# Optimization experiments

Measured on AMD Instinct MI355X. Metric: run time of the kernel, lower is better.

## Reference

```python
import jax, jax.numpy as jnp
import numpy as np

B, N, C_IN, FC0, K = 16, 32768, 32, 256, 1024
CHUNK = 64  # chunk over the K=1024 attention channels to bound the [N,CHUNK,C] intermediate
BN_EPS = 1e-5


def _lengths():
    rng = np.random.default_rng(0)
    r = rng.integers(1024, 3072, size=B)
    l = (r * N) // r.sum()
    l[-1] += N - l.sum()
    assert l.min() > 0 and l.sum() == N
    return jnp.asarray(l, dtype=jnp.int32)


def setup_inputs() -> dict:
    key = jax.random.key(0)
    ks = jax.random.split(key, 16)
    f32 = jnp.float32
    x = jax.random.normal(ks[0], (N, C_IN), dtype=f32)
    # conv1d_1 (1x1 conv == per-point linear), BN1
    w1 = jax.random.normal(ks[1], (FC0, C_IN), dtype=f32) * 0.1
    b1 = jax.random.normal(ks[2], (FC0,), dtype=f32) * 0.1
    g1 = 1.0 + 0.1 * jax.random.normal(ks[3], (FC0,), dtype=f32)
    be1 = 0.1 * jax.random.normal(ks[4], (FC0,), dtype=f32)
    m1 = 0.1 * jax.random.normal(ks[5], (FC0,), dtype=f32)
    v1 = 0.5 + jax.random.uniform(ks[6], (FC0,), dtype=f32)
    # conv1d_2, BN2
    w2 = jax.random.normal(ks[7], (K, FC0), dtype=f32) * 0.05
    b2 = jax.random.normal(ks[8], (K,), dtype=f32) * 0.1
    g2 = 1.0 + 0.1 * jax.random.normal(ks[9], (K,), dtype=f32)
    be2 = 0.1 * jax.random.normal(ks[10], (K,), dtype=f32)
    m2 = 0.1 * jax.random.normal(ks[11], (K,), dtype=f32)
    v2 = 0.5 + jax.random.uniform(ks[12], (K,), dtype=f32)
    # fc_1, BN3
    fcw = jax.random.normal(ks[13], (FC0, C_IN * K), dtype=f32) * 0.01
    fcb = jax.random.normal(ks[14], (FC0,), dtype=f32) * 0.1
    kb = jax.random.split(ks[15], 4)
    g3 = 1.0 + 0.1 * jax.random.normal(kb[0], (FC0,), dtype=f32)
    be3 = 0.1 * jax.random.normal(kb[1], (FC0,), dtype=f32)
    m3 = 0.1 * jax.random.normal(kb[2], (FC0,), dtype=f32)
    v3 = 0.5 + jax.random.uniform(kb[3], (FC0,), dtype=f32)
    return dict(x=x, length=_lengths(), w1=w1, b1=b1, g1=g1, be1=be1, m1=m1, v1=v1,
                w2=w2, b2=b2, g2=g2, be2=be2, m2=m2, v2=v2,
                fcw=fcw, fcb=fcb, g3=g3, be3=be3, m3=m3, v3=v3)


def _bn(x, g, b, m, v):
    # eval-mode BatchNorm (running stats)
    return (x - m) * (g * jax.lax.rsqrt(v + BN_EPS)) + b


def _forward(x, length, w1, b1, g1, be1, m1, v1, w2, b2, g2, be2, m2, v2,
             fcw, fcb, g3, be3, m3, v3):
    # attention features: conv1x1 -> BN -> ReLU, twice  -> [N, K]
    att = jax.nn.relu(_bn(x @ w1.T + b1, g1, be1, m1, v1))
    att = jax.nn.relu(_bn(att @ w2.T + b2, g2, be2, m2, v2))

    seg = jnp.repeat(jnp.arange(B, dtype=jnp.int32), length, total_repeat_length=N)  # [N]

    # per-segment softmax over the point axis (torch F.softmax(..., dim=0))
    mx = jax.ops.segment_max(att, seg, num_segments=B)              # [B, K]
    e = jnp.exp(att - mx[seg])
    w = e / jax.ops.segment_sum(e, seg, num_segments=B)[seg]        # [N, K]

    # per-segment weighted pooling: out[b] = att_b.T @ x_b, chunked over K
    chunks = []
    for s in range(0, K, CHUNK):
        contrib = w[:, s:s + CHUNK, None] * x[:, None, :]           # [N, CHUNK, C]
        chunks.append(jax.ops.segment_sum(contrib, seg, num_segments=B))
    pooled = jnp.concatenate(chunks, axis=1)                        # [B, K, C]
    pooled = pooled / length[:, None, None].astype(x.dtype)
    out2 = pooled.reshape(B, K * C_IN)                              # row-major flatten of [K, C]

    r = _bn(out2 @ fcw.T + fcb, g3, be3, m3, v3)                    # [B, 256]
    # F.normalize(p=2, dim=1, eps=1e-12)
    return r / jnp.maximum(jnp.linalg.norm(r, axis=1, keepdims=True), 1e-12)


def reference(x, length, w1, b1, g1, be1, m1, v1, w2, b2, g2, be2, m2, v2,
              fcw, fcb, g3, be3, m3, v3):
    return _forward(x, length, w1, b1, g1, be1, m1, v1, w2, b2, g2, be2, m2, v2,
                    fcw, fcb, g3, be3, m3, v3)
```

## Files before the change

### kernel.cpp

```cpp
#include <hip/hip_runtime.h>
#include <hip/hip_bf16.h>

typedef __bf16 bf16x8 __attribute__((ext_vector_type(8)));
typedef unsigned short u16x8 __attribute__((ext_vector_type(8)));
typedef float f32x4 __attribute__((ext_vector_type(4)));
typedef unsigned long long ull;

__device__ inline unsigned short f2bf(float f) {
    unsigned u = __builtin_bit_cast(unsigned, f);
    unsigned r = (u + 0x7fffu + ((u >> 16) & 1u)) >> 16;
    return (unsigned short)r;
}
__device__ inline float bf2f(unsigned short h) {
    unsigned u = ((unsigned)h) << 16;
    return __builtin_bit_cast(float, u);
}

__device__ inline void gload_lds16(const void* g, void* l) {
    __builtin_amdgcn_global_load_lds((const __attribute__((address_space(1))) void*)g,
                                     (__attribute__((address_space(3))) void*)l, 16, 0, 0);
}

#define MAXCH 272

__global__ __launch_bounds__(256) void k01_prep_gemm1(const float* __restrict__ x,
                                                      const float* __restrict__ w1,
                                                      const float* __restrict__ b1,
                                                      const float* __restrict__ g1,
                                                      const float* __restrict__ be1,
                                                      const float* __restrict__ m1,
                                                      const float* __restrict__ v1,
                                                      const float* __restrict__ w2,
                                                      const int* __restrict__ length,
                                                      unsigned short* __restrict__ w2p,
                                                      int* __restrict__ meta,
                                                      unsigned short* __restrict__ att1) {
    int tid = threadIdx.x;
    int i = blockIdx.x * 256 + tid;
    if (i < 32768) {
        int kb = i >> 9, kk = (i >> 6) & 7, l = i & 63;
        int col = kb * 16 + (l & 15);
        int kin = kk * 32 + (l >> 4) * 8;
        unsigned short v[8];
#pragma unroll
        for (int j = 0; j < 8; j++) v[j] = f2bf(w2[(size_t)col * 256 + kin + j]);
        *(ull*)(w2p + (size_t)i * 8)     = *(ull*)&v[0];
        *(ull*)(w2p + (size_t)i * 8 + 4) = *(ull*)&v[4];
    }
    if (blockIdx.x == 0 && tid < 64) {
        int lane = tid;
        int b = lane & 15;
        int len = length[b];
        int off = 0, chbase = 0, nch = 0;
        int nchb = (len + 127) >> 7;
#pragma unroll
        for (int j = 0; j < 16; j++) {
            int lj = __shfl(len, j, 64);
            int nj = __shfl(nchb, j, 64);
            if (j < b) { off += lj; chbase += nj; }
            nch += nj;
        }
        int total = __shfl(off + len, 15, 64);
        if (lane < 16) {
            meta[b] = off;
            meta[848 + b] = chbase;
            meta[864 + b] = chbase + nchb;
            if (b == 0) { meta[16] = total; meta[17] = nch; }
            for (int t = 0; t < nchb; t++) {
                int s = off + t * 128;
                int en = off + len < s + 128 ? off + len : s + 128;
                meta[304 + chbase + t] = s;
                meta[576 + chbase + t] = en;
            }
        }
    }
    __shared__ float xs[64][33];
    int row0 = blockIdx.x * 64;
    for (int ii = tid; ii < 64 * 32; ii += 256) {
        int rr = ii >> 5, c = ii & 31;
        xs[rr][c] = x[(row0 + rr) * 32 + c];
    }
    __syncthreads();
    int j = tid;
    float w[32];
#pragma unroll
    for (int c = 0; c < 32; c++) w[c] = w1[j * 32 + c];
    float s = g1[j] * rsqrtf(v1[j] + 1e-5f);
    float bias = (b1[j] - m1[j]) * s + be1[j];
    for (int rr = 0; rr < 64; rr++) {
        float acc = 0.f;
#pragma unroll
        for (int c = 0; c < 32; c++) acc = fmaf(xs[rr][c], w[c], acc);
        float t = fmaf(acc, s, bias);
        att1[(row0 + rr) * 256 + j] = f2bf(fmaxf(t, 0.f));
    }
}

__global__ __launch_bounds__(256, 2) void k23_fused(const unsigned short* __restrict__ att1,
                                                    const unsigned short* __restrict__ w2p,
                                                    const float* __restrict__ x,
                                                    const int* __restrict__ meta,
                                                    const float* __restrict__ b2,
                                                    const float* __restrict__ g2,
                                                    const float* __restrict__ be2,
                                                    const float* __restrict__ m2,
                                                    const float* __restrict__ v2,
                                                    unsigned short* __restrict__ pP,
                                                    float* __restrict__ pS) {
    __shared__ __align__(16) unsigned short As[2][128 * 64];
    __shared__ __align__(16) unsigned short xT[48 * 128];
    int flat = blockIdx.x;
    int xcd = flat & 7, q = flat >> 3;
    int ch = (q >> 3) * 8 + xcd;
    int kt = q & 7;
    if (ch >= meta[17]) return;
    int n0 = meta[304 + ch];
    int rows = meta[576 + ch] - n0;
    int col0 = kt * 128;
    int tid = threadIdx.x, lane = tid & 63, wave = tid >> 6;
    int lr = lane & 15, s16 = lane >> 4;
    int wr = wave >> 1, wc = wave & 1;

    auto stage = [&](int t, int buf) {
#pragma unroll
        for (int it = 0; it < 4; it++) {
            int idx = it * 256 + tid;
            int row = idx >> 3, slot = idx & 7;
            int srow = row < rows ? row : rows - 1;
            int g = slot ^ (row & 7);
            gload_lds16(att1 + (size_t)(n0 + srow) * 256 + t * 64 + g * 8,
                        (char*)As + buf * 16384 + it * 4096 + wave * 1024);
        }
    };

    int kb0 = kt * 8 + wc * 4;
    auto loadB = [&](int t, bf16x8 (&bb)[2][4]) {
#pragma unroll
        for (int kk = 0; kk < 2; kk++)
#pragma unroll
            for (int n = 0; n < 4; n++)
                bb[kk][n] = *(const bf16x8*)(const void*)(
                    w2p + (size_t)(((kb0 + n) * 8 + t * 2 + kk) * 64 + lane) * 8);
    };

    bf16x8 b0[2][4], b1[2][4];
    stage(0, 0);
    loadB(0, b0);

#pragma unroll
    for (int p = 0; p < 8; p++) {
        int nb = p * 16 + (tid >> 5) * 2;
        int c = tid & 31;
        float v0 = (nb < rows) ? x[(size_t)(n0 + nb) * 32 + c] : 0.f;
        float v1 = (nb + 1 < rows) ? x[(size_t)(n0 + nb + 1) * 32 + c] : 0.f;
        unsigned pk = ((unsigned)f2bf(v1) << 16) | f2bf(v0);
        int byte = c * 256 + ((nb * 2) ^ ((c & 15) << 4));
        *(unsigned*)((char*)xT + byte) = pk;
    }
    if (tid < 128) {
        int byte = 32 * 256 + tid * 2;
        *(unsigned short*)((char*)xT + byte) = (tid < rows) ? f2bf(1.f) : (unsigned short)0;
    }
    __syncthreads();

    f32x4 acc[4][4] = {};
#pragma unroll
    for (int t = 0; t < 4; t++) {
        if (t < 3) stage(t + 1, (t & 1) ^ 1);
        if (t == 0) loadB(1, b1);
        else if (t == 1) loadB(2, b0);
        else if (t == 2) loadB(3, b1);
        const char* Ab = (const char*)As + (t & 1) * 16384;
#pragma unroll
        for (int kk = 0; kk < 2; kk++) {
            bf16x8 a[4];
#pragma unroll
            for (int m = 0; m < 4; m++) {
                int row = wr * 64 + m * 16 + lr;
                int slot = (kk * 4 + s16) ^ (row & 7);
                a[m] = *(const bf16x8*)(const void*)(Ab + row * 128 + slot * 16);
            }
#pragma unroll
            for (int m = 0; m < 4; m++)
#pragma unroll
                for (int n = 0; n < 4; n++)
                    acc[m][n] = __builtin_amdgcn_mfma_f32_16x16x32_bf16(
                        a[m], (t & 1) ? b1[kk][n] : b0[kk][n], acc[m][n], 0, 0, 0);
        }
        __syncthreads();
    }

    char* eT = (char*)As;
#pragma unroll
    for (int nf = 0; nf < 4; nf++) {
        int k = wc * 64 + nf * 16 + lr;
        int kg = col0 + k;
        float sc = g2[kg] * rsqrtf(v2[kg] + 1e-5f);
        float bias = (b2[kg] - m2[kg]) * sc + be2[kg];
#pragma unroll
        for (int m = 0; m < 4; m++) {
            int nbase = wr * 64 + m * 16 + s16 * 4;
            ull pk = 0;
#pragma unroll
            for (int rg = 0; rg < 4; rg++) {
                float tt = fmaf(acc[m][nf][rg], sc, bias);
                float ev = __expf(fmaxf(tt, 0.f));
                unsigned short h = (nbase + rg < rows) ? f2bf(ev) : (unsigned short)0;
                pk |= ((ull)h) << (16 * rg);
            }
            int byte = k * 256 + ((nbase * 2) ^ ((k & 15) << 4));
            *(ull*)(eT + byte) = pk;
        }
    }
    __syncthreads();

    f32x4 pacc[2][3] = {};
#pragma unroll
    for (int nc = 0; nc < 128; nc += 32) {
        bf16x8 ea[2], xb[3];
#pragma unroll
        for (int i = 0; i < 2; i++) {
            int k = (wave * 2 + i) * 16 + lr;
            int byte = k * 256 + (((nc + s16 * 8) * 2) ^ ((k & 15) << 4));
            ea[i] = *(const bf16x8*)(const void*)(eT + byte);
        }
#pragma unroll
        for (int j = 0; j < 3; j++) {
            int c = j * 16 + lr;
            int byte = c * 256 + (((nc + s16 * 8) * 2) ^ ((c & 15) << 4));
            xb[j] = *(const bf16x8*)(const void*)((const char*)xT + byte);
        }
#pragma unroll
        for (int i = 0; i < 2; i++)
#pragma unroll
            for (int j = 0; j < 3; j++)
                pacc[i][j] = __builtin_amdgcn_mfma_f32_16x16x32_bf16(ea[i], xb[j], pacc[i][j], 0, 0, 0);
    }

    unsigned short* pPc = pP + (size_t)ch * 32768;
#pragma unroll
    for (int i = 0; i < 2; i++) {
#pragma unroll
        for (int j = 0; j < 3; j++) {
            int c = j * 16 + lr;
#pragma unroll
            for (int rg = 0; rg < 4; rg++) {
                int k = (wave * 2 + i) * 16 + s16 * 4 + rg;
                float v = pacc[i][j][rg];
                if (c < 32) pPc[(col0 + k) * 32 + c] = f2bf(v);
                else if (c == 32) pS[ch * 1024 + col0 + k] = v;
            }
        }
    }
}

__global__ __launch_bounds__(256) void k3b_reduce(const unsigned short* __restrict__ pP,
                                                  const float* __restrict__ pS,
                                                  const int* __restrict__ meta,
                                                  float* __restrict__ out2) {
    int id = blockIdx.x * 256 + threadIdx.x;
    int base = id * 8;
    int b = base >> 15, rem = base & 32767, k = rem >> 5;
    float P[8] = {};
    float S = 0.f;
    int c0 = meta[848 + b], c1 = meta[864 + b];
    for (int ch = c0; ch < c1; ch++) {
        u16x8 v = *(const u16x8*)(const void*)(pP + (size_t)ch * 32768 + rem);
#pragma unroll
        for (int j = 0; j < 8; j++) P[j] += bf2f(v[j]);
        S += pS[ch * 1024 + k];
    }
    float inv = 1.f / (S * (float)(meta[b + 1] - meta[b]));
    f32x4 o0 = {P[0] * inv, P[1] * inv, P[2] * inv, P[3] * inv};
    f32x4 o1 = {P[4] * inv, P[5] * inv, P[6] * inv, P[7] * inv};
    *(f32x4*)(void*)(out2 + base) = o0;
    *(f32x4*)(void*)(out2 + base + 4) = o1;
}

__global__ __launch_bounds__(256) void k4_fc(const float* __restrict__ out2,
                                             const float* __restrict__ fcw,
                                             float* __restrict__ pFC) {
    int jt = blockIdx.x, dc = blockIdx.y;
    int tid = threadIdx.x;
    float acc[16][8] = {};
#pragma unroll
    for (int i = 0; i < 8; i++) {
        int d = dc * 2048 + i * 256 + tid;
        float wv[8];
#pragma unroll
        for (int jj = 0; jj < 8; jj++) wv[jj] = fcw[(size_t)(jt * 8 + jj) * 32768 + d];
#pragma unroll
        for (int bb = 0; bb < 16; bb++) {
            float ov = out2[bb * 32768 + d];
#pragma unroll
            for (int jj = 0; jj < 8; jj++) acc[bb][jj] = fmaf(ov, wv[jj], acc[bb][jj]);
        }
    }
    __shared__ float red[32][257];
#pragma unroll
    for (int p = 0; p < 4; p++) {
#pragma unroll
        for (int q = 0; q < 4; q++)
#pragma unroll
            for (int jj = 0; jj < 8; jj++)
                red[q * 8 + jj][tid] = acc[p * 4 + q][jj];
        __syncthreads();
        int row = tid >> 3, sg = tid & 7;
        float s = 0.f;
        for (int u = sg; u < 256; u += 8) s += red[row][u];
        s += __shfl_down(s, 4, 8);
        s += __shfl_down(s, 2, 8);
        s += __shfl_down(s, 1, 8);
        if (sg == 0) {
            int bb = p * 4 + (row >> 3), jj = row & 7;
            pFC[(dc * 16 + bb) * 256 + jt * 8 + jj] = s;
        }
        __syncthreads();
    }
}

__global__ __launch_bounds__(256) void k45_fc2(const float* __restrict__ pFC,
                                               const float* __restrict__ fcb,
                                               const float* __restrict__ g3,
                                               const float* __restrict__ be3,
                                               const float* __restrict__ m3,
                                               const float* __restrict__ v3,
                                               float* __restrict__ out) {
    int b = blockIdx.x, j = threadIdx.x;
    float sum = 0.f;
#pragma unroll
    for (int dc = 0; dc < 16; dc++) sum += pFC[(dc * 16 + b) * 256 + j];
    float sc = g3[j] * rsqrtf(v3[j] + 1e-5f);
    float rv = (sum + fcb[j] - m3[j]) * sc + be3[j];
    float sq = rv * rv;
#pragma unroll
    for (int o = 32; o > 0; o >>= 1) sq += __shfl_down(sq, o, 64);
    __shared__ float wsum[4];
    if ((j & 63) == 0) wsum[j >> 6] = sq;
    __syncthreads();
    float tot = wsum[0] + wsum[1] + wsum[2] + wsum[3];
    out[b * 256 + j] = rv / fmaxf(sqrtf(tot), 1e-12f);
}

extern "C" void kernel_launch(void* const* d_in, const int* in_sizes, int n_in,
                              void* d_out, int out_size, void* d_ws, size_t ws_size,
                              hipStream_t stream) {
    const float* x    = (const float*)d_in[0];
    const int*   len  = (const int*)d_in[1];
    const float* w1   = (const float*)d_in[2];
    const float* b1   = (const float*)d_in[3];
    const float* g1   = (const float*)d_in[4];
    const float* be1  = (const float*)d_in[5];
    const float* m1   = (const float*)d_in[6];
    const float* v1   = (const float*)d_in[7];
    const float* w2   = (const float*)d_in[8];
    const float* b2   = (const float*)d_in[9];
    const float* g2   = (const float*)d_in[10];
    const float* be2  = (const float*)d_in[11];
    const float* m2   = (const float*)d_in[12];
    const float* v2   = (const float*)d_in[13];
    const float* fcw  = (const float*)d_in[14];
    const float* fcb  = (const float*)d_in[15];
    const float* g3   = (const float*)d_in[16];
    const float* be3  = (const float*)d_in[17];
    const float* m3   = (const float*)d_in[18];
    const float* v3   = (const float*)d_in[19];

    char* ws = (char*)d_ws;
    int* meta            = (int*)ws;
    unsigned short* w2p  = (unsigned short*)(ws + 4096);
    unsigned short* att1 = (unsigned short*)(ws + 528384);
    unsigned short* pP   = (unsigned short*)(ws + 17305600);
    float* pS            = (float*)(ws + 35131392);
    float* out2          = (float*)(ws + 36245504);
    float* pFC           = (float*)(ws + 38342656);
    float* out           = (float*)d_out;

    hipLaunchKernelGGL(k01_prep_gemm1, dim3(512),   dim3(256), 0, stream,
                       x, w1, b1, g1, be1, m1, v1, w2, len, w2p, meta, att1);
    hipLaunchKernelGGL(k23_fused,  dim3(MAXCH * 8), dim3(256), 0, stream, att1, w2p, x, meta, b2, g2, be2, m2, v2, pP, pS);
    hipLaunchKernelGGL(k3b_reduce, dim3(256),       dim3(256), 0, stream, pP, pS, meta, out2);
    hipLaunchKernelGGL(k4_fc,      dim3(32, 16),    dim3(256), 0, stream, out2, fcw, pFC);
    hipLaunchKernelGGL(k45_fc2,    dim3(16),        dim3(256), 0, stream, pFC, fcb, g3, be3, m3, v3, out);
}
```

Before: 92.38 us.

## Use MFMA for first pointwise GEMM and halve per-thread work in reduce

The first 1x1 conv GEMM (x @ w1^T) moves from scalar FMA loops to bf16 MFMA 16x16x32 instructions. Results are staged through LDS so att1 can be written with coalesced 16-byte stores. The partial-sum reduce kernel now has each thread handle 4 outputs instead of 8, doubling the grid to 512 blocks for more parallelism. Rounding x and w1 to bf16 before the GEMM adds precision loss.

```diff
diff --git a/kernel.cpp b/kernel.cpp
--- a/kernel.cpp
+++ b/kernel.cpp
@@ -2,6 +2,7 @@
 #include <hip/hip_bf16.h>
 
 typedef __bf16 bf16x8 __attribute__((ext_vector_type(8)));
+typedef unsigned short u16x4 __attribute__((ext_vector_type(4)));
 typedef unsigned short u16x8 __attribute__((ext_vector_type(8)));
 typedef float f32x4 __attribute__((ext_vector_type(4)));
 typedef unsigned long long ull;
@@ -35,6 +36,7 @@
                                                       unsigned short* __restrict__ w2p,
                                                       int* __restrict__ meta,
                                                       unsigned short* __restrict__ att1) {
+    __shared__ __align__(16) unsigned short st[64 * 256];
     int tid = threadIdx.x;
     int i = blockIdx.x * 256 + tid;
     if (i < 32768) {
@@ -74,25 +76,60 @@
             }
         }
     }
-    __shared__ float xs[64][33];
     int row0 = blockIdx.x * 64;
-    for (int ii = tid; ii < 64 * 32; ii += 256) {
-        int rr = ii >> 5, c = ii & 31;
-        xs[rr][c] = x[(row0 + rr) * 32 + c];
+    int lane = tid & 63, wave = tid >> 6;
+    int lr = lane & 15, s16 = lane >> 4;
+
+    bf16x8 a[4], b[4];
+#pragma unroll
+    for (int m = 0; m < 4; m++) {
+        const float* xp = x + (size_t)(row0 + m * 16 + lr) * 32 + s16 * 8;
+        f32x4 lo = *(const f32x4*)(const void*)xp;
+        f32x4 hi = *(const f32x4*)(const void*)(xp + 4);
+        unsigned short v[8];
+#pragma unroll
+        for (int j = 0; j < 4; j++) { v[j] = f2bf(lo[j]); v[4 + j] = f2bf(hi[j]); }
+        a[m] = *(bf16x8*)v;
+    }
+#pragma unroll
+    for (int n = 0; n < 4; n++) {
+        const float* wp = w1 + (size_t)(wave * 64 + n * 16 + lr) * 32 + s16 * 8;
+        f32x4 lo = *(const f32x4*)(const void*)wp;
+        f32x4 hi = *(const f32x4*)(const void*)(wp + 4);
+        unsigned short v[8];
+#pragma unroll
+        for (int j = 0; j < 4; j++) { v[j] = f2bf(lo[j]); v[4 + j] = f2bf(hi[j]); }
+        b[n] = *(bf16x8*)v;
+    }
+    f32x4 acc[4][4] = {};
+#pragma unroll
+    for (int m = 0; m < 4; m++)
+#pragma unroll
+        for (int n = 0; n < 4; n++)
+            acc[m][n] = __builtin_amdgcn_mfma_f32_16x16x32_bf16(a[m], b[n], acc[m][n], 0, 0, 0);
+
+    int cc = lane & 15, cr4 = (lane >> 4) * 4;
+#pragma unroll
+    for (int n = 0; n < 4; n++) {
+        int j = wave * 64 + n * 16 + cc;
+        float s = g1[j] * rsqrtf(v1[j] + 1e-5f);
+        float bias = (b1[j] - m1[j]) * s + be1[j];
+#pragma unroll
+        for (int m = 0; m < 4; m++) {
+#pragma unroll
+            for (int rg = 0; rg < 4; rg++) {
+                int rl = m * 16 + cr4 + rg;
+                float t = fmaf(acc[m][n][rg], s, bias);
+                st[rl * 256 + j] = f2bf(fmaxf(t, 0.f));
+            }
+        }
     }
     __syncthreads();
-    int j = tid;
-    float w[32];
-#pragma unroll
-    for (int c = 0; c < 32; c++) w[c] = w1[j * 32 + c];
-    float s = g1[j] * rsqrtf(v1[j] + 1e-5f);
-    float bias = (b1[j] - m1[j]) * s + be1[j];
-    for (int rr = 0; rr < 64; rr++) {
-        float acc = 0.f;
-#pragma unroll
-        for (int c = 0; c < 32; c++) acc = fmaf(xs[rr][c], w[c], acc);
-        float t = fmaf(acc, s, bias);
-        att1[(row0 + rr) * 256 + j] = f2bf(fmaxf(t, 0.f));
+#pragma unroll
+    for (int p = 0; p < 8; p++) {
+        int idx = p * 256 + tid;
+        *(f32x4*)(void*)(att1 + (size_t)row0 * 256 + idx * 8) =
+            *(const f32x4*)(const void*)((const char*)st + idx * 16);
     }
 }
 
@@ -259,22 +296,20 @@
                                                   const int* __restrict__ meta,
                                                   float* __restrict__ out2) {
     int id = blockIdx.x * 256 + threadIdx.x;
-    int base = id * 8;
+    int base = id * 4;
     int b = base >> 15, rem = base & 32767, k = rem >> 5;
-    float P[8] = {};
+    float P[4] = {};
     float S = 0.f;
     int c0 = meta[848 + b], c1 = meta[864 + b];
     for (int ch = c0; ch < c1; ch++) {
-        u16x8 v = *(const u16x8*)(const void*)(pP + (size_t)ch * 32768 + rem);
-#pragma unroll
-        for (int j = 0; j < 8; j++) P[j] += bf2f(v[j]);
+        u16x4 v = *(const u16x4*)(const void*)(pP + (size_t)ch * 32768 + rem);
+#pragma unroll
+        for (int j = 0; j < 4; j++) P[j] += bf2f(v[j]);
         S += pS[ch * 1024 + k];
     }
     float inv = 1.f / (S * (float)(meta[b + 1] - meta[b]));
-    f32x4 o0 = {P[0] * inv, P[1] * inv, P[2] * inv, P[3] * inv};
-    f32x4 o1 = {P[4] * inv, P[5] * inv, P[6] * inv, P[7] * inv};
-    *(f32x4*)(void*)(out2 + base) = o0;
-    *(f32x4*)(void*)(out2 + base + 4) = o1;
+    f32x4 o = {P[0] * inv, P[1] * inv, P[2] * inv, P[3] * inv};
+    *(f32x4*)(void*)(out2 + base) = o;
 }
 
 __global__ __launch_bounds__(256) void k4_fc(const float* __restrict__ out2,
@@ -379,7 +414,7 @@
     hipLaunchKernelGGL(k01_prep_gemm1, dim3(512),   dim3(256), 0, stream,
                        x, w1, b1, g1, be1, m1, v1, w2, len, w2p, meta, att1);
     hipLaunchKernelGGL(k23_fused,  dim3(MAXCH * 8), dim3(256), 0, stream, att1, w2p, x, meta, b2, g2, be2, m2, v2, pP, pS);
-    hipLaunchKernelGGL(k3b_reduce, dim3(256),       dim3(256), 0, stream, pP, pS, meta, out2);
+    hipLaunchKernelGGL(k3b_reduce, dim3(512),       dim3(256), 0, stream, pP, pS, meta, out2);
     hipLaunchKernelGGL(k4_fc,      dim3(32, 16),    dim3(256), 0, stream, out2, fcw, pFC);
     hipLaunchKernelGGL(k45_fc2,    dim3(16),        dim3(256), 0, stream, pFC, fcb, g3, be3, m3, v3, out);
 }
```

After: 78.86 us, median of 3. 1.17x faster.
